# Kernel optimization log

Measured on AMD Instinct MI355X. Metric: run time of the kernel, lower is better.

The kernel has to match this reference:

```python
import jax, jax.numpy as jnp
import numpy as np

TOP_K = 30
NUM_RBF = 16
MAX_REL = 32          # max_relative_feature
EDGE_FEATURES = 128
NUM_POS_EMB = 16
EDGE_INS = NUM_POS_EMB + NUM_RBF * 25  # 416
ONEHOT_DIM = 2 * MAX_REL + 2           # 66

# 25 (A, B) atom-pair indices into stacked order [Ca, N, C, O, Cb]
PAIR_A = np.array([0,1,2,3,4, 0,0,0,0, 1,1,1, 4,4, 3, 1,2,3,4, 2,3,4, 2,3, 2])
PAIR_B = np.array([0,1,2,3,4, 1,2,3,4, 2,3,4, 2,3, 2, 0,0,0,0, 1,1,1, 4,4, 3])


def setup_inputs() -> dict:
    key = jax.random.key(0)
    k1, k2, k3, k4, k5 = jax.random.split(key, 5)
    B, L = 4, 2048
    X = jax.random.normal(k1, (B, L, 4, 3), dtype=jnp.float32)
    mask = jnp.ones((B, L), dtype=jnp.float32)
    residue_idx = jnp.arange(B * L, dtype=jnp.int64 if jax.config.jax_enable_x64 else jnp.int32).reshape(B, L)
    # parameters
    W_pos = jax.random.normal(k2, (ONEHOT_DIM, NUM_POS_EMB), dtype=jnp.float32) * 0.02
    b_pos = jnp.zeros((NUM_POS_EMB,), dtype=jnp.float32)
    W_edge = jax.random.normal(k3, (EDGE_INS, EDGE_FEATURES), dtype=jnp.float32) * 0.02
    ln_gamma = jnp.ones((EDGE_FEATURES,), dtype=jnp.float32)
    ln_beta = jnp.zeros((EDGE_FEATURES,), dtype=jnp.float32)
    return {"X": X, "mask": mask, "residue_idx": residue_idx,
            "W_pos": W_pos, "b_pos": b_pos, "W_edge": W_edge,
            "ln_gamma": ln_gamma, "ln_beta": ln_beta}


def reference(X, mask, residue_idx, W_pos, b_pos, W_edge, ln_gamma, ln_beta):
    eps = 1e-6
    Bsz, L = X.shape[0], X.shape[1]
    K = min(TOP_K, L)

    # virtual Cb construction
    b = X[:, :, 1, :] - X[:, :, 0, :]
    c = X[:, :, 2, :] - X[:, :, 1, :]
    a = jnp.cross(b, c)
    Cb = -0.58273431 * a + 0.56802827 * b - 0.54067466 * c + X[:, :, 1, :]
    Ca = X[:, :, 1, :]
    N_ = X[:, :, 0, :]
    C_ = X[:, :, 2, :]
    O_ = X[:, :, 3, :]

    # --- _dist on Ca: masked pairwise distance + top-k smallest ---
    mask2d = mask[:, None, :] * mask[:, :, None]              # [B, L, L]
    dX = Ca[:, :, None, :] - Ca[:, None, :, :]                # [B, L, L, 3]
    D = mask2d * jnp.sqrt(jnp.sum(dX * dX, axis=-1) + eps)    # [B, L, L]
    D_max = jnp.max(D, axis=-1, keepdims=True)
    D_adjust = D + (1.0 - mask2d) * D_max
    neg_vals, E_idx = jax.lax.top_k(-D_adjust, K)             # smallest-k, ascending

    # --- 25 atom-pair distances, gathered only at neighbor indices ---
    atoms = jnp.stack([Ca, N_, C_, O_, Cb], axis=0)           # [5, B, L, 3]
    A_all = atoms[PAIR_A]                                     # [25, B, L, 3]
    B_all = atoms[PAIR_B]                                     # [25, B, L, 3]
    # gather neighbor coords: [25, B, L, K, 3]
    gather_b = jax.vmap(lambda coords, idx: coords[idx], in_axes=(0, 0))      # over batch
    gather_pb = jax.vmap(gather_b, in_axes=(0, None))                         # over pairs
    B_nb = gather_pb(B_all, E_idx)
    diff = A_all[:, :, :, None, :] - B_nb
    D_nb = jnp.sqrt(jnp.sum(diff * diff, axis=-1) + 1e-6)     # [25, B, L, K]

    # --- RBF featurization ---
    D_mu = jnp.linspace(2.0, 22.0, NUM_RBF, dtype=D_nb.dtype)
    D_sigma = (22.0 - 2.0) / NUM_RBF
    RBF = jnp.exp(-(((D_nb[..., None] - D_mu) / D_sigma) ** 2))  # [25, B, L, K, R]
    # concat order: [B, L, K, 25*R]
    RBF_all = jnp.transpose(RBF, (1, 2, 3, 0, 4)).reshape(Bsz, L, K, 25 * NUM_RBF)

    # --- relative positional encodings ---
    offset = residue_idx[:, :, None] - residue_idx[:, None, :]    # [B, L, L]
    off_nb = jnp.take_along_axis(offset, E_idx, axis=2)           # [B, L, K]
    d = jnp.clip(off_nb + MAX_REL, 0, 2 * MAX_REL)
    d_onehot = jax.nn.one_hot(d, ONEHOT_DIM, dtype=W_pos.dtype)   # [B, L, K, 66]
    E_pos = d_onehot @ W_pos + b_pos                              # [B, L, K, 16]

    # --- edge embedding + layernorm ---
    E = jnp.concatenate([E_pos, RBF_all], axis=-1)                # [B, L, K, 416]
    E = E @ W_edge                                                # [B, L, K, 128]
    mu = jnp.mean(E, axis=-1, keepdims=True)
    var = jnp.mean((E - mu) ** 2, axis=-1, keepdims=True)
    E = (E - mu) / jnp.sqrt(var + 1e-5) * ln_gamma + ln_beta
    return E
```

## Files before the change

kernel.cpp:

```cpp
#include <hip/hip_runtime.h>
#include <hip/hip_bf16.h>
#include <math.h>

#define BB      4
#define LL      2048
#define KNB     30
#define NRES    (BB*LL)
#define NEDGE   (NRES*KNB)
#define EDGE_IN 416
#define KT      13
#define KTA     7
#define ME      32
#define AST2    232
#define FINF    3.4e38f
#define LOG2E   1.44269504088896340736f

typedef __attribute__((ext_vector_type(8))) _Float16 half8;
typedef __attribute__((ext_vector_type(4))) float floatx4;

__device__ __constant__ int d_PA[25] = {0,1,2,3,4,0,0,0,0,1,1,1,4,4,3,1,2,3,4,2,3,4,2,3,2};
__device__ __constant__ int d_PB[25] = {0,1,2,3,4,1,2,3,4,2,3,4,2,3,2,0,0,0,0,1,1,1,4,4,3};

__device__ __forceinline__ unsigned short f2h_bits(float x) {
    _Float16 h = (_Float16)x;
    union { _Float16 h; unsigned short u; } v; v.h = h;
    return v.u;
}
__device__ __forceinline__ unsigned pack2h(float a, float b) {
    return (unsigned)f2h_bits(a) | ((unsigned)f2h_bits(b) << 16);
}

__global__ __launch_bounds__(256) void atoms_kernel(const float* __restrict__ X,
                                                    float* __restrict__ atoms,
                                                    float* __restrict__ caTx,
                                                    float* __restrict__ caTy,
                                                    float* __restrict__ caTz) {
    int r = blockIdx.x * blockDim.x + threadIdx.x;
    if (r >= NRES) return;
    const float* xr = X + (size_t)r * 12;
    float Nx = xr[0],  Ny = xr[1],  Nz = xr[2];
    float Ax = xr[3],  Ay = xr[4],  Az = xr[5];
    float Cx = xr[6],  Cy = xr[7],  Cz = xr[8];
    float Ox = xr[9],  Oy = xr[10], Oz = xr[11];
    float bx = Ax - Nx, by = Ay - Ny, bz = Az - Nz;
    float cx = Cx - Ax, cy = Cy - Ay, cz = Cz - Az;
    float ax = by * cz - bz * cy;
    float ay = bz * cx - bx * cz;
    float az = bx * cy - by * cx;
    float Cbx = -0.58273431f * ax + 0.56802827f * bx - 0.54067466f * cx + Ax;
    float Cby = -0.58273431f * ay + 0.56802827f * by - 0.54067466f * cy + Ay;
    float Cbz = -0.58273431f * az + 0.56802827f * bz - 0.54067466f * cz + Az;
    float* o = atoms + (size_t)r * 15;
    o[0]  = Ax;  o[1]  = Ay;  o[2]  = Az;
    o[3]  = Nx;  o[4]  = Ny;  o[5]  = Nz;
    o[6]  = Cx;  o[7]  = Cy;  o[8]  = Cz;
    o[9]  = Ox;  o[10] = Oy;  o[11] = Oz;
    o[12] = Cbx; o[13] = Cby; o[14] = Cbz;
    caTx[r] = Ax; caTy[r] = Ay; caTz[r] = Az;
}

__global__ __launch_bounds__(256) void topk_kernel(const float* __restrict__ caTx,
                                                   const float* __restrict__ caTy,
                                                   const float* __restrict__ caTz,
                                                   const float* __restrict__ mask,
                                                   int* __restrict__ E_idx) {
#pragma clang fp contract(off)
    __shared__ float Dv[4][LL];

    int t    = threadIdx.x;
    int wid  = t >> 6;
    int lane = t & 63;
    int bi   = blockIdx.x * 4 + wid;
    int b    = bi >> 11;
    int j0   = b << 11;

    float cx = caTx[bi], cy = caTy[bi], cz = caTz[bi];
    float mi = mask[bi];
    float* dv = Dv[wid];

    float aa[32];
    float lmax = 0.0f;
#pragma unroll
    for (int i = 0; i < 32; i++) {
        int j = j0 + i * 64 + lane;
        float dx = cx - caTx[j], dy = cy - caTy[j], dz = cz - caTz[j];
        float ssq = ((dx * dx + dy * dy) + dz * dz) + 1e-6f;
        float m2  = mask[j] * mi;
        float Dj  = m2 * sqrtf(ssq);
        aa[i] = Dj;
        lmax = fmaxf(lmax, Dj);
    }
    for (int off = 32; off; off >>= 1) lmax = fmaxf(lmax, __shfl_xor(lmax, off));

    float l0 = FINF, l1 = FINF, l2 = FINF, l3 = FINF;
    int   i0 = 0,    i1 = 0,    i2 = 0,    i3 = 0;
#pragma unroll
    for (int i = 0; i < 32; i++) {
        float m2 = mask[j0 + i * 64 + lane] * mi;
        float v  = aa[i] + (1.0f - m2) * lmax;
        dv[i * 64 + lane] = v;
        bool c0 = v < l0, c1 = v < l1, c2 = v < l2, c3 = v < l3;
        l3 = c2 ? l2 : (c3 ? v : l3);  i3 = c2 ? i2 : (c3 ? i : i3);
        l2 = c1 ? l1 : (c2 ? v : l2);  i2 = c1 ? i1 : (c2 ? i : i2);
        l1 = c0 ? l0 : (c1 ? v : l1);  i1 = c0 ? i0 : (c1 ? i : i1);
        l0 = c0 ? v  : l0;             i0 = c0 ? i  : i0;
    }

    int* outp = E_idx + (size_t)bi * KNB;
#pragma unroll 1
    for (int r = 0; r < KNB; r++) {
        float bv = l0;
        int   bj = (i0 << 6) | lane;
        for (int off = 1; off < 64; off <<= 1) {
            float ov = __shfl_xor(bv, off);
            int   oj = __shfl_xor(bj, off);
            if (ov < bv || (ov == bv && oj < bj)) { bv = ov; bj = oj; }
        }
        if (lane == 0) outp[r] = bj;
        bool mine = ((bj & 63) == lane);
        if (mine) {
            dv[bj] = FINF;
            l0 = l1; i0 = i1;
            l1 = l2; i1 = i2;
            l2 = l3; i2 = i3;
            l3 = FINF;
        }
        bool need = mine && (l0 == FINF) && (r < KNB - 1);
        if (need) {
            l0 = FINF; l1 = FINF; l2 = FINF; l3 = FINF;
            i0 = 0; i1 = 0; i2 = 0; i3 = 0;
#pragma unroll
            for (int i = 0; i < 32; i++) {
                float v = dv[i * 64 + lane];
                bool c0 = v < l0, c1 = v < l1, c2 = v < l2, c3 = v < l3;
                l3 = c2 ? l2 : (c3 ? v : l3);  i3 = c2 ? i2 : (c3 ? i : i3);
                l2 = c1 ? l1 : (c2 ? v : l2);  i2 = c1 ? i1 : (c2 ? i : i2);
                l1 = c0 ? l0 : (c1 ? v : l1);  i1 = c0 ? i0 : (c1 ? i : i1);
                l0 = c0 ? v  : l0;             i0 = c0 ? i  : i0;
            }
        }
    }
}

__global__ __launch_bounds__(256) void wprep_kernel(const float* __restrict__ W_edge,
                                                    half8* __restrict__ Wfh,
                                                    half8* __restrict__ Wfl) {
    int t = blockIdx.x * blockDim.x + threadIdx.x;
    if (t >= KT * 8 * 64) return;
    int kk   = t >> 9;
    int rem  = t & 511;
    int nt   = rem >> 6;
    int lane = rem & 63;
    int n  = nt * 16 + (lane & 15);
    int kb = kk * 32 + (lane >> 4) * 8;
    half8 vh, vl;
#pragma unroll
    for (int j = 0; j < 8; j++) {
        float w = W_edge[(size_t)(kb + j) * 128 + n];
        _Float16 wh = (_Float16)w;
        vh[j] = wh;
        vl[j] = (_Float16)(w - (float)wh);
    }
    Wfh[t] = vh;
    Wfl[t] = vl;
}

__global__ __launch_bounds__(256) void edge_kernel(const float* __restrict__ atoms,
                                                   const int* __restrict__ E_idx,
                                                   const int* __restrict__ resi,
                                                   const float* __restrict__ W_pos,
                                                   const float* __restrict__ b_pos,
                                                   const half8* __restrict__ Wfh,
                                                   const half8* __restrict__ Wfl,
                                                   const float* __restrict__ gamma,
                                                   const float* __restrict__ beta,
                                                   float* __restrict__ out) {
    __shared__ _Float16 Ah[ME * AST2];
    __shared__ _Float16 Al[ME * AST2];
    __shared__ float Dl[ME][26];
    __shared__ float redS[2][ME];
    __shared__ int   s_gi[ME], s_gj[ME], s_d[ME];

    int t  = threadIdx.x;
    int e0 = blockIdx.x * ME;

    if (t < ME) {
        int e  = e0 + t;
        int gi = e / KNB;
        int k  = e - gi * KNB;
        int b  = gi >> 11;
        int j  = E_idx[(size_t)gi * KNB + k];
        s_gi[t] = gi;
        s_gj[t] = (b << 11) + j;
        int off = resi[gi] - resi[(b << 11) + j];
        int d = off + 32;
        s_d[t] = d < 0 ? 0 : (d > 64 ? 64 : d);
    }
    __syncthreads();

    for (int idx = t; idx < ME * 25; idx += 256) {
        int e = idx / 25, p = idx - e * 25;
        const float* Ar = atoms + (size_t)s_gi[e] * 15 + d_PA[p] * 3;
        const float* Br = atoms + (size_t)s_gj[e] * 15 + d_PB[p] * 3;
        float dx = Ar[0] - Br[0];
        float dy = Ar[1] - Br[1];
        float dz = Ar[2] - Br[2];
        Dl[e][p] = sqrtf(dx * dx + dy * dy + dz * dz + 1e-6f);
    }
    __syncthreads();

    {
        int e  = t >> 3;
        int j8 = t & 7;
        const float* dle = Dl[e];
        _Float16* ah = &Ah[e * AST2];
        _Float16* al = &Al[e * AST2];
        if (j8 < 4) {
            int c = j8 * 4;
            int dpos = s_d[e];
            const float* wp = W_pos + dpos * 16 + c;
            float v[4];
#pragma unroll
            for (int q = 0; q < 4; q++) v[q] = wp[q] + b_pos[c + q];
            float h0 = (float)(_Float16)v[0], h1 = (float)(_Float16)v[1];
            float h2 = (float)(_Float16)v[2], h3 = (float)(_Float16)v[3];
            *(unsigned*)&ah[c + 0] = pack2h(v[0], v[1]);
            *(unsigned*)&ah[c + 2] = pack2h(v[2], v[3]);
            *(unsigned*)&al[c + 0] = pack2h(v[0] - h0, v[1] - h1);
            *(unsigned*)&al[c + 2] = pack2h(v[2] - h2, v[3] - h3);
        }
#pragma unroll
        for (int i = 0; i < 13; i++) {
            int c2 = 2 * (j8 + 8 * i);
            int p  = c2 >> 4;
            int r  = c2 & 15;
            float D = dle[p];
            float mu0 = 2.0f + (float)r * (20.0f / 15.0f);
            float mu1 = 2.0f + (float)(r + 1) * (20.0f / 15.0f);
            float t0 = (D - mu0) * 0.8f;
            float t1 = (D - mu1) * 0.8f;
            float g0 = __builtin_amdgcn_exp2f(-(t0 * t0) * LOG2E);
            float g1 = __builtin_amdgcn_exp2f(-(t1 * t1) * LOG2E);
            float h0 = (float)(_Float16)g0, h1 = (float)(_Float16)g1;
            *(unsigned*)&ah[16 + c2] = pack2h(g0, g1);
            *(unsigned*)&al[16 + c2] = pack2h(g0 - h0, g1 - h1);
        }
    }
    __syncthreads();

    int lane  = t & 63;
    int w     = t >> 6;
    int strip = (w & 1) * 16;
    int h     = w >> 1;
    int m     = lane & 15;
    int quad  = lane >> 4;
    const _Float16* pah = &Ah[(strip + m) * AST2 + quad * 8];
    const _Float16* pal = &Al[(strip + m) * AST2 + quad * 8];

    floatx4 acc[4];
#pragma unroll
    for (int c = 0; c < 4; c++) acc[c] = (floatx4){0.f, 0.f, 0.f, 0.f};

    half8 bh[4], bl[4], bnh[4], bnl[4];
#pragma unroll
    for (int c = 0; c < 4; c++) {
        int idx = (h * 4 + c) * 64 + lane;
        bh[c] = Wfh[idx];
        bl[c] = Wfl[idx];
    }

#pragma unroll 1
    for (int kk = 0; kk < KTA; kk++) {
        half8 a_hi = *(const half8*)(pah + kk * 32);
        half8 a_lo = *(const half8*)(pal + kk * 32);
#pragma unroll
        for (int c = 0; c < 4; c++) {
            int idx = ((kk + 1) * 8 + h * 4 + c) * 64 + lane;
            bnh[c] = Wfh[idx];
            bnl[c] = Wfl[idx];
        }
#pragma unroll
        for (int c = 0; c < 4; c++) {
            acc[c] = __builtin_amdgcn_mfma_f32_16x16x32_f16(a_hi, bh[c], acc[c], 0, 0, 0);
            acc[c] = __builtin_amdgcn_mfma_f32_16x16x32_f16(a_lo, bh[c], acc[c], 0, 0, 0);
            acc[c] = __builtin_amdgcn_mfma_f32_16x16x32_f16(a_hi, bl[c], acc[c], 0, 0, 0);
        }
#pragma unroll
        for (int c = 0; c < 4; c++) { bh[c] = bnh[c]; bl[c] = bnl[c]; }
    }

    __syncthreads();

    {
        int e  = t >> 3;
        int j8 = t & 7;
        const float* dle = Dl[e];
        _Float16* ah = &Ah[e * AST2];
        _Float16* al = &Al[e * AST2];
#pragma unroll
        for (int i = 13; i < 25; i++) {
            int c2 = 2 * (j8 + 8 * i);
            int p  = c2 >> 4;
            int r  = c2 & 15;
            float D = dle[p];
            float mu0 = 2.0f + (float)r * (20.0f / 15.0f);
            float mu1 = 2.0f + (float)(r + 1) * (20.0f / 15.0f);
            float t0 = (D - mu0) * 0.8f;
            float t1 = (D - mu1) * 0.8f;
            float g0 = __builtin_amdgcn_exp2f(-(t0 * t0) * LOG2E);
            float g1 = __builtin_amdgcn_exp2f(-(t1 * t1) * LOG2E);
            float h0 = (float)(_Float16)g0, h1 = (float)(_Float16)g1;
            int col = c2 - 208;
            *(unsigned*)&ah[col] = pack2h(g0, g1);
            *(unsigned*)&al[col] = pack2h(g0 - h0, g1 - h1);
        }
    }
    __syncthreads();

#pragma unroll 1
    for (int kk = KTA; kk < KT; kk++) {
        half8 a_hi = *(const half8*)(pah + (kk - KTA) * 32);
        half8 a_lo = *(const half8*)(pal + (kk - KTA) * 32);
        if (kk < KT - 1) {
#pragma unroll
            for (int c = 0; c < 4; c++) {
                int idx = ((kk + 1) * 8 + h * 4 + c) * 64 + lane;
                bnh[c] = Wfh[idx];
                bnl[c] = Wfl[idx];
            }
        }
#pragma unroll
        for (int c = 0; c < 4; c++) {
            acc[c] = __builtin_amdgcn_mfma_f32_16x16x32_f16(a_hi, bh[c], acc[c], 0, 0, 0);
            acc[c] = __builtin_amdgcn_mfma_f32_16x16x32_f16(a_lo, bh[c], acc[c], 0, 0, 0);
            acc[c] = __builtin_amdgcn_mfma_f32_16x16x32_f16(a_hi, bl[c], acc[c], 0, 0, 0);
        }
#pragma unroll
        for (int c = 0; c < 4; c++) { bh[c] = bnh[c]; bl[c] = bnl[c]; }
    }

    int elb = strip + quad * 4;
    float sarr[4];
#pragma unroll
    for (int r = 0; r < 4; r++) {
        float s = acc[0][r] + acc[1][r] + acc[2][r] + acc[3][r];
        for (int msk = 1; msk <= 8; msk <<= 1) s += __shfl_xor(s, msk);
        sarr[r] = s;
    }
    if (m == 0) {
#pragma unroll
        for (int r = 0; r < 4; r++) redS[h][elb + r] = sarr[r];
    }
    __syncthreads();
    float mu[4];
#pragma unroll
    for (int r = 0; r < 4; r++) mu[r] = (redS[0][elb + r] + redS[1][elb + r]) * (1.0f / 128.0f);
    __syncthreads();
    float dvv[4][4];
#pragma unroll
    for (int r = 0; r < 4; r++) {
        float v = 0.f;
#pragma unroll
        for (int c = 0; c < 4; c++) { dvv[c][r] = acc[c][r] - mu[r]; v += dvv[c][r] * dvv[c][r]; }
        for (int msk = 1; msk <= 8; msk <<= 1) v += __shfl_xor(v, msk);
        if (m == 0) redS[h][elb + r] = v;
    }
    __syncthreads();
#pragma unroll
    for (int r = 0; r < 4; r++) {
        float var  = (redS[0][elb + r] + redS[1][elb + r]) * (1.0f / 128.0f);
        float rstd = rsqrtf(var + 1e-5f);
        int e = e0 + elb + r;
        float* orow = out + (size_t)e * 128;
#pragma unroll
        for (int c = 0; c < 4; c++) {
            int n = (h * 4 + c) * 16 + m;
            orow[n] = dvv[c][r] * rstd * gamma[n] + beta[n];
        }
    }
}

extern "C" void kernel_launch(void* const* d_in, const int* in_sizes, int n_in,
                              void* d_out, int out_size, void* d_ws, size_t ws_size,
                              hipStream_t stream) {
    const float* X      = (const float*)d_in[0];
    const float* mask   = (const float*)d_in[1];
    const int*   resi   = (const int*)  d_in[2];
    const float* W_pos  = (const float*)d_in[3];
    const float* b_pos  = (const float*)d_in[4];
    const float* W_edge = (const float*)d_in[5];
    const float* gamma  = (const float*)d_in[6];
    const float* beta   = (const float*)d_in[7];
    float* out = (float*)d_out;

    float* atoms = (float*)d_ws;
    int*   E_idx = (int*)((char*)d_ws + (size_t)NRES * 15 * 4);
    half8* Wfh   = (half8*)((char*)d_ws + 1474560);
    half8* Wfl   = (half8*)((char*)d_ws + 1581056);
    float* caTx  = (float*)((char*)d_ws + 1687552);
    float* caTy  = (float*)((char*)d_ws + 1720320);
    float* caTz  = (float*)((char*)d_ws + 1753088);

    atoms_kernel<<<(NRES + 255) / 256, 256, 0, stream>>>(X, atoms, caTx, caTy, caTz);
    wprep_kernel<<<(KT * 8 * 64 + 255) / 256, 256, 0, stream>>>(W_edge, Wfh, Wfl);
    topk_kernel<<<NRES / 4, 256, 0, stream>>>(caTx, caTy, caTz, mask, E_idx);
    edge_kernel<<<NEDGE / ME, 256, 0, stream>>>(atoms, E_idx, resi,
                                                W_pos, b_pos, Wfh, Wfl, gamma, beta, out);
}
```

Baseline: 321.3 us.

## Drop topk shared distance buffer and split edge A-tile into three stages

```diff
diff --git a/kernel.cpp b/kernel.cpp
--- a/kernel.cpp
+++ b/kernel.cpp
@@ -9,9 +9,8 @@
 #define NEDGE   (NRES*KNB)
 #define EDGE_IN 416
 #define KT      13
-#define KTA     7
 #define ME      32
-#define AST2    232
+#define AST3    168
 #define FINF    3.4e38f
 #define LOG2E   1.44269504088896340736f
 
@@ -59,14 +58,12 @@
     caTx[r] = Ax; caTy[r] = Ay; caTz[r] = Az;
 }
 
-__global__ __launch_bounds__(256) void topk_kernel(const float* __restrict__ caTx,
-                                                   const float* __restrict__ caTy,
-                                                   const float* __restrict__ caTz,
-                                                   const float* __restrict__ mask,
-                                                   int* __restrict__ E_idx) {
+__global__ __launch_bounds__(256, 6) void topk_kernel(const float* __restrict__ caTx,
+                                                      const float* __restrict__ caTy,
+                                                      const float* __restrict__ caTz,
+                                                      const float* __restrict__ mask,
+                                                      int* __restrict__ E_idx) {
 #pragma clang fp contract(off)
-    __shared__ float Dv[4][LL];
-
     int t    = threadIdx.x;
     int wid  = t >> 6;
     int lane = t & 63;
@@ -76,7 +73,6 @@
 
     float cx = caTx[bi], cy = caTy[bi], cz = caTz[bi];
     float mi = mask[bi];
-    float* dv = Dv[wid];
 
     float aa[32];
     float lmax = 0.0f;
@@ -98,7 +94,7 @@
     for (int i = 0; i < 32; i++) {
         float m2 = mask[j0 + i * 64 + lane] * mi;
         float v  = aa[i] + (1.0f - m2) * lmax;
-        dv[i * 64 + lane] = v;
+        aa[i] = v;
         bool c0 = v < l0, c1 = v < l1, c2 = v < l2, c3 = v < l3;
         l3 = c2 ? l2 : (c3 ? v : l3);  i3 = c2 ? i2 : (c3 ? i : i3);
         l2 = c1 ? l1 : (c2 ? v : l2);  i2 = c1 ? i1 : (c2 ? i : i2);
@@ -106,6 +102,7 @@
         l0 = c0 ? v  : l0;             i0 = c0 ? i  : i0;
     }
 
+    unsigned consumed = 0;
     int* outp = E_idx + (size_t)bi * KNB;
 #pragma unroll 1
     for (int r = 0; r < KNB; r++) {
@@ -119,7 +116,7 @@
         if (lane == 0) outp[r] = bj;
         bool mine = ((bj & 63) == lane);
         if (mine) {
-            dv[bj] = FINF;
+            consumed |= 1u << ((unsigned)bj >> 6);
             l0 = l1; i0 = i1;
             l1 = l2; i1 = i2;
             l2 = l3; i2 = i3;
@@ -131,7 +128,7 @@
             i0 = 0; i1 = 0; i2 = 0; i3 = 0;
 #pragma unroll
             for (int i = 0; i < 32; i++) {
-                float v = dv[i * 64 + lane];
+                float v = (consumed & (1u << i)) ? FINF : aa[i];
                 bool c0 = v < l0, c1 = v < l1, c2 = v < l2, c3 = v < l3;
                 l3 = c2 ? l2 : (c3 ? v : l3);  i3 = c2 ? i2 : (c3 ? i : i3);
                 l2 = c1 ? l1 : (c2 ? v : l2);  i2 = c1 ? i1 : (c2 ? i : i2);
@@ -175,8 +172,8 @@
                                                    const float* __restrict__ gamma,
                                                    const float* __restrict__ beta,
                                                    float* __restrict__ out) {
-    __shared__ _Float16 Ah[ME * AST2];
-    __shared__ _Float16 Al[ME * AST2];
+    __shared__ _Float16 Ah[ME * AST3];
+    __shared__ _Float16 Al[ME * AST3];
     __shared__ float Dl[ME][26];
     __shared__ float redS[2][ME];
     __shared__ int   s_gi[ME], s_gj[ME], s_d[ME];
@@ -209,29 +206,30 @@
     }
     __syncthreads();
 
+    int fe  = t >> 3;
+    int fj8 = t & 7;
+    const float* dle = Dl[fe];
+    _Float16* fah = &Ah[fe * AST3];
+    _Float16* fal = &Al[fe * AST3];
+
     {
-        int e  = t >> 3;
-        int j8 = t & 7;
-        const float* dle = Dl[e];
-        _Float16* ah = &Ah[e * AST2];
-        _Float16* al = &Al[e * AST2];
-        if (j8 < 4) {
-            int c = j8 * 4;
-            int dpos = s_d[e];
+        if (fj8 < 4) {
+            int c = fj8 * 4;
+            int dpos = s_d[fe];
             const float* wp = W_pos + dpos * 16 + c;
             float v[4];
 #pragma unroll
             for (int q = 0; q < 4; q++) v[q] = wp[q] + b_pos[c + q];
             float h0 = (float)(_Float16)v[0], h1 = (float)(_Float16)v[1];
             float h2 = (float)(_Float16)v[2], h3 = (float)(_Float16)v[3];
-            *(unsigned*)&ah[c + 0] = pack2h(v[0], v[1]);
-            *(unsigned*)&ah[c + 2] = pack2h(v[2], v[3]);
-            *(unsigned*)&al[c + 0] = pack2h(v[0] - h0, v[1] - h1);
-            *(unsigned*)&al[c + 2] = pack2h(v[2] - h2, v[3] - h3);
-        }
-#pragma unroll
-        for (int i = 0; i < 13; i++) {
-            int c2 = 2 * (j8 + 8 * i);
+            *(unsigned*)&fah[c + 0] = pack2h(v[0], v[1]);
+            *(unsigned*)&fah[c + 2] = pack2h(v[2], v[3]);
+            *(unsigned*)&fal[c + 0] = pack2h(v[0] - h0, v[1] - h1);
+            *(unsigned*)&fal[c + 2] = pack2h(v[2] - h2, v[3] - h3);
+        }
+#pragma unroll
+        for (int i = 0; i < 9; i++) {
+            int c2 = 2 * (fj8 + 8 * i);
             int p  = c2 >> 4;
             int r  = c2 & 15;
             float D = dle[p];
@@ -242,8 +240,8 @@
             float g0 = __builtin_amdgcn_exp2f(-(t0 * t0) * LOG2E);
             float g1 = __builtin_amdgcn_exp2f(-(t1 * t1) * LOG2E);
             float h0 = (float)(_Float16)g0, h1 = (float)(_Float16)g1;
-            *(unsigned*)&ah[16 + c2] = pack2h(g0, g1);
-            *(unsigned*)&al[16 + c2] = pack2h(g0 - h0, g1 - h1);
+            *(unsigned*)&fah[16 + c2] = pack2h(g0, g1);
+            *(unsigned*)&fal[16 + c2] = pack2h(g0 - h0, g1 - h1);
         }
     }
     __syncthreads();
@@ -254,8 +252,8 @@
     int h     = w >> 1;
     int m     = lane & 15;
     int quad  = lane >> 4;
-    const _Float16* pah = &Ah[(strip + m) * AST2 + quad * 8];
-    const _Float16* pal = &Al[(strip + m) * AST2 + quad * 8];
+    const _Float16* pah = &Ah[(strip + m) * AST3 + quad * 8];
+    const _Float16* pal = &Al[(strip + m) * AST3 + quad * 8];
 
     floatx4 acc[4];
 #pragma unroll
@@ -270,7 +268,7 @@
     }
 
 #pragma unroll 1
-    for (int kk = 0; kk < KTA; kk++) {
+    for (int kk = 0; kk < 5; kk++) {
         half8 a_hi = *(const half8*)(pah + kk * 32);
         half8 a_lo = *(const half8*)(pal + kk * 32);
 #pragma unroll
@@ -292,14 +290,9 @@
     __syncthreads();
 
     {
-        int e  = t >> 3;
-        int j8 = t & 7;
-        const float* dle = Dl[e];
-        _Float16* ah = &Ah[e * AST2];
-        _Float16* al = &Al[e * AST2];
-#pragma unroll
-        for (int i = 13; i < 25; i++) {
-            int c2 = 2 * (j8 + 8 * i);
+#pragma unroll
+        for (int i = 9; i < 17; i++) {
+            int c2 = 2 * (fj8 + 8 * i);
             int p  = c2 >> 4;
             int r  = c2 & 15;
             float D = dle[p];
@@ -310,17 +303,60 @@
             float g0 = __builtin_amdgcn_exp2f(-(t0 * t0) * LOG2E);
             float g1 = __builtin_amdgcn_exp2f(-(t1 * t1) * LOG2E);
             float h0 = (float)(_Float16)g0, h1 = (float)(_Float16)g1;
-            int col = c2 - 208;
-            *(unsigned*)&ah[col] = pack2h(g0, g1);
-            *(unsigned*)&al[col] = pack2h(g0 - h0, g1 - h1);
+            int col = c2 - 144;
+            *(unsigned*)&fah[col] = pack2h(g0, g1);
+            *(unsigned*)&fal[col] = pack2h(g0 - h0, g1 - h1);
         }
     }
     __syncthreads();
 
 #pragma unroll 1
-    for (int kk = KTA; kk < KT; kk++) {
-        half8 a_hi = *(const half8*)(pah + (kk - KTA) * 32);
-        half8 a_lo = *(const half8*)(pal + (kk - KTA) * 32);
+    for (int kk = 5; kk < 9; kk++) {
+        half8 a_hi = *(const half8*)(pah + (kk - 5) * 32);
+        half8 a_lo = *(const half8*)(pal + (kk - 5) * 32);
+#pragma unroll
+        for (int c = 0; c < 4; c++) {
+            int idx = ((kk + 1) * 8 + h * 4 + c) * 64 + lane;
+            bnh[c] = Wfh[idx];
+            bnl[c] = Wfl[idx];
+        }
+#pragma unroll
+        for (int c = 0; c < 4; c++) {
+            acc[c] = __builtin_amdgcn_mfma_f32_16x16x32_f16(a_hi, bh[c], acc[c], 0, 0, 0);
+            acc[c] = __builtin_amdgcn_mfma_f32_16x16x32_f16(a_lo, bh[c], acc[c], 0, 0, 0);
+            acc[c] = __builtin_amdgcn_mfma_f32_16x16x32_f16(a_hi, bl[c], acc[c], 0, 0, 0);
+        }
+#pragma unroll
+        for (int c = 0; c < 4; c++) { bh[c] = bnh[c]; bl[c] = bnl[c]; }
+    }
+
+    __syncthreads();
+
+    {
+#pragma unroll
+        for (int i = 17; i < 25; i++) {
+            int c2 = 2 * (fj8 + 8 * i);
+            int p  = c2 >> 4;
+            int r  = c2 & 15;
+            float D = dle[p];
+            float mu0 = 2.0f + (float)r * (20.0f / 15.0f);
+            float mu1 = 2.0f + (float)(r + 1) * (20.0f / 15.0f);
+            float t0 = (D - mu0) * 0.8f;
+            float t1 = (D - mu1) * 0.8f;
+            float g0 = __builtin_amdgcn_exp2f(-(t0 * t0) * LOG2E);
+            float g1 = __builtin_amdgcn_exp2f(-(t1 * t1) * LOG2E);
+            float h0 = (float)(_Float16)g0, h1 = (float)(_Float16)g1;
+            int col = c2 - 272;
+            *(unsigned*)&fah[col] = pack2h(g0, g1);
+            *(unsigned*)&fal[col] = pack2h(g0 - h0, g1 - h1);
+        }
+    }
+    __syncthreads();
+
+#pragma unroll 1
+    for (int kk = 9; kk < KT; kk++) {
+        half8 a_hi = *(const half8*)(pah + (kk - 9) * 32);
+        half8 a_lo = *(const half8*)(pal + (kk - 9) * 32);
         if (kk < KT - 1) {
 #pragma unroll
             for (int c = 0; c < 4; c++) {
```

New measurement: 320.7 us. No clear change (-0.2%).
